# Kernel optimization log

Measured on AMD Instinct MI355X. Metric: run time of the kernel, lower is better.

## Reference

```python
import jax, jax.numpy as jnp
import numpy as np

# --- static config (matches init_kwargs) ---
B = 2; HI = 60; WI = 60; T = 4; WS = 8; SHIFT = 4
C = 256; NH = 8; HD = C // NH; HID = 1024
P = HI * WI; N = T * P
PAD = (WS - HI % WS) % WS           # 4 -> pad 60 -> 64
HP = HI + PAD; WP = WI + PAD
NWH = HP // WS; NWW = WP // WS
L = WS * WS                          # 64 tokens per window
SCALE = HD ** -0.5

# relative position index [L, L] (constant)
_c = np.stack(np.meshgrid(np.arange(WS), np.arange(WS), indexing='ij')).reshape(2, -1)
_r = (_c[:, :, None] - _c[:, None, :]).transpose(1, 2, 0) + WS - 1
REL_IDX = jnp.asarray(_r[..., 0] * (2 * WS - 1) + _r[..., 1])

# per-window key padding mask [nWin, L] (True = padded token)
_b = np.zeros((HP, WP), bool); _b[HI:, :] = True; _b[:, WI:] = True
WIN_MASK = jnp.asarray(_b.reshape(NWH, WS, NWW, WS).transpose(0, 2, 1, 3).reshape(NWH * NWW, L))


def _ln(x, w, b):
    m = x.mean(-1, keepdims=True)
    v = jnp.square(x - m).mean(-1, keepdims=True)
    return (x - m) * jax.lax.rsqrt(v + 1e-5) * w + b


def _partition(x4):  # [Bm, HP, WP, C] -> [Bm*nWin, L, C]
    Bm = x4.shape[0]
    return x4.reshape(Bm, NWH, WS, NWW, WS, C).transpose(0, 1, 3, 2, 4, 5).reshape(Bm * NWH * NWW, L, C)


def _win_attn(xq, xkv, qw, qb, kw, kb, vw, vb, ow, ob, bias_table):
    Bm = B * T
    q4 = xq.reshape(Bm, HI, WI, C)
    k4 = xkv.reshape(Bm, HI, WI, C)
    q4 = jnp.roll(q4, (-SHIFT, -SHIFT), (1, 2))
    k4 = jnp.roll(k4, (-SHIFT, -SHIFT), (1, 2))
    pad = ((0, 0), (0, PAD), (0, PAD), (0, 0))
    q4 = jnp.pad(q4, pad); k4 = jnp.pad(k4, pad)
    q_win = _partition(q4)   # [Bw, L, C]
    kv_win = _partition(k4)
    q = (q_win @ qw.T + qb).reshape(-1, L, NH, HD)
    k = (kv_win @ kw.T + kb).reshape(-1, L, NH, HD)
    v = (kv_win @ vw.T + vb).reshape(-1, L, NH, HD)
    attn = jnp.einsum('bihd,bjhd->bhij', q, k) * SCALE
    attn = attn + bias_table[REL_IDX].transpose(2, 0, 1)[None]      # RPB [1,H,L,L]
    km = jnp.tile(WIN_MASK, (Bm, 1))                                  # [Bw, L]
    attn = jnp.where(km[:, None, None, :], -jnp.inf, attn)
    p = jax.nn.softmax(attn, axis=-1)
    o = jnp.einsum('bhij,bjhd->bihd', p, v).reshape(-1, L, C)
    o = o @ ow.T + ob
    y = o.reshape(Bm, NWH, NWW, WS, WS, C).transpose(0, 1, 3, 2, 4, 5).reshape(Bm, HP, WP, C)
    y = y[:, :HI, :WI, :]
    y = jnp.roll(y, (SHIFT, SHIFT), (1, 2))
    return y.reshape(B, N, C)


def reference(x, context, ln1_w, ln1_b, ln2_w, ln2_b, ln3_w, ln3_b, lnc_w, lnc_b,
              sa_q_w, sa_q_b, sa_k_w, sa_k_b, sa_v_w, sa_v_b, sa_o_w, sa_o_b, sa_bias,
              ca_q_w, ca_q_b, ca_k_w, ca_k_b, ca_v_w, ca_v_b, ca_o_w, ca_o_b, ca_bias,
              gamma1, gamma2, gamma_mlp, mlp_w1, mlp_b1, mlp_w2, mlp_b2):
    xn = _ln(x, ln1_w, ln1_b)
    y_s = _win_attn(xn, xn, sa_q_w, sa_q_b, sa_k_w, sa_k_b, sa_v_w, sa_v_b, sa_o_w, sa_o_b, sa_bias)
    x = x + gamma1 * y_s
    y_c = _win_attn(_ln(x, ln2_w, ln2_b), _ln(context, lnc_w, lnc_b),
                    ca_q_w, ca_q_b, ca_k_w, ca_k_b, ca_v_w, ca_v_b, ca_o_w, ca_o_b, ca_bias)
    x = x + gamma2 * y_c
    h = _ln(x, ln3_w, ln3_b)
    h = jax.nn.gelu(h @ mlp_w1.T + mlp_b1, approximate=False) @ mlp_w2.T + mlp_b2
    return x + gamma_mlp * h


def setup_inputs() -> dict:
    key = jax.random.key(0)
    ks = jax.random.split(key, 16)
    def w(k, shape, s=0.02):
        return jax.random.normal(k, shape, jnp.float32) * s
    inp = {}
    inp['x'] = jax.random.normal(ks[0], (B, N, C), jnp.float32)
    inp['context'] = jax.random.normal(ks[1], (B, N, C), jnp.float32)
    for nm in ['ln1', 'ln2', 'ln3', 'lnc']:
        inp[f'{nm}_w'] = jnp.ones((C,), jnp.float32)
        inp[f'{nm}_b'] = jnp.zeros((C,), jnp.float32)
    i = 2
    for pfx in ['sa', 'ca']:
        for pn in ['q', 'k', 'v', 'o']:
            inp[f'{pfx}_{pn}_w'] = w(ks[i], (C, C)); i += 1
            inp[f'{pfx}_{pn}_b'] = jnp.zeros((C,), jnp.float32)
        inp[f'{pfx}_bias'] = w(ks[i], ((2 * WS - 1) * (2 * WS - 1), NH)); i += 1
    inp['gamma1'] = jnp.ones((1,), jnp.float32)
    inp['gamma2'] = jnp.ones((1,), jnp.float32)
    inp['gamma_mlp'] = jnp.full((1,), 0.1, jnp.float32)
    inp['mlp_w1'] = w(ks[i], (HID, C)); i += 1
    inp['mlp_b1'] = jnp.zeros((HID,), jnp.float32)
    inp['mlp_w2'] = w(ks[i], (C, HID)); i += 1
    inp['mlp_b2'] = jnp.zeros((C,), jnp.float32)
    return inp
```

## Files before the change

kernel.cpp:

```cpp
#include <hip/hip_runtime.h>
#include <math.h>

#define BN    28800
#define CC    256
#define HIDN  1024
#define WINS  512
#define WROWS (WINS*64)
#define ATT_SCALE 0.1767766952966369f

typedef __bf16 bf16x8 __attribute__((ext_vector_type(8)));
typedef float  f32x4  __attribute__((ext_vector_type(4)));

__device__ __forceinline__ unsigned short f2bf(float f) {
    unsigned u = __float_as_uint(f);
    unsigned r = (u + 0x7FFFu + ((u >> 16) & 1u)) >> 16;
    return (unsigned short)r;
}
__device__ __forceinline__ float bf2f(unsigned short u) {
    return __uint_as_float((unsigned)u << 16);
}

__device__ __forceinline__ float gelu_f(float x) {
    float x3 = x * x * x;
    float e  = __expf(1.5957691216057308f * (x + 0.044715f * x3));
    float th = 1.0f - 2.0f * __builtin_amdgcn_rcpf(e + 1.0f);
    return 0.5f * x * (1.0f + th);
}

__device__ __forceinline__ void gl_lds16(const void* g, void* l) {
    __builtin_amdgcn_global_load_lds(
        (const __attribute__((address_space(1))) void*)g,
        (__attribute__((address_space(3))) void*)l, 16, 0, 0);
}

__global__ void ln_gather(const float* __restrict__ x, const float* __restrict__ w,
                          const float* __restrict__ b, unsigned short* __restrict__ dst) {
    int row  = (int)((blockIdx.x * blockDim.x + threadIdx.x) >> 6);
    int lane = threadIdx.x & 63;
    if (row >= WROWS) return;
    int win = row >> 6, l = row & 63;
    int f   = win >> 6;
    int wih = (win >> 3) & 7, wiw = win & 7;
    int r = l >> 3, s = l & 7;
    int h = wih * 8 + r, wc = wiw * 8 + s;
    if (h >= 60 || wc >= 60) {
        ushort4 z = {0, 0, 0, 0};
        reinterpret_cast<ushort4*>(dst + (size_t)row * CC)[lane] = z;
        return;
    }
    int oh = (h + 4) % 60, ow = (wc + 4) % 60;
    size_t tok = (size_t)f * 3600 + (size_t)oh * 60 + ow;
    float4 v = reinterpret_cast<const float4*>(x + tok * CC)[lane];
    float sm  = v.x + v.y + v.z + v.w;
    float s2 = v.x*v.x + v.y*v.y + v.z*v.z + v.w*v.w;
#pragma unroll
    for (int off = 32; off >= 1; off >>= 1) {
        sm += __shfl_xor(sm, off);
        s2 += __shfl_xor(s2, off);
    }
    float mean = sm * (1.0f / CC);
    float var  = s2 * (1.0f / CC) - mean * mean;
    float rs   = rsqrtf(var + 1e-5f);
    float4 wv = reinterpret_cast<const float4*>(w)[lane];
    float4 bv = reinterpret_cast<const float4*>(b)[lane];
    ushort4 o;
    o.x = f2bf((v.x - mean) * rs * wv.x + bv.x);
    o.y = f2bf((v.y - mean) * rs * wv.y + bv.y);
    o.z = f2bf((v.z - mean) * rs * wv.z + bv.z);
    o.w = f2bf((v.w - mean) * rs * wv.w + bv.w);
    reinterpret_cast<ushort4*>(dst + (size_t)row * CC)[lane] = o;
}

template <bool GELU, int FUSE, int TN>
__global__ __launch_bounds__(512, 4) void gemm_wa(
        const unsigned short* __restrict__ Wt,
        const unsigned short* __restrict__ Act,
        const float* __restrict__ b0, const float* __restrict__ b1,
        const float* __restrict__ b2, const float* __restrict__ b3,
        unsigned short* __restrict__ o0, unsigned short* __restrict__ o1,
        unsigned short* __restrict__ o2, unsigned short* __restrict__ o3,
        int strideO, int vseg, int K, int Ntok,
        const float* __restrict__ xres, const float* __restrict__ gammap,
        float* __restrict__ fout) {
    constexpr int NW   = TN / 64;
    constexpr int BP   = TN / 128;
    constexpr int BUFB = 8192 + TN * 64;
    constexpr int POOLB = (3 * BUFB > TN * 256) ? 3 * BUFB : TN * 256;
    __shared__ __align__(16) char pool[POOLB];
    unsigned short* Cs = (unsigned short*)pool;

    const int t = threadIdx.x;
    const int w = t >> 6;
    const int l = t & 63;
    const int Mb = gridDim.x;
    int lin = blockIdx.y * Mb + blockIdx.x;
    int T = Mb * gridDim.y;
    int q = T >> 3, rr = T & 7;
    int xcd = lin & 7, slot = lin >> 3;
    int wid = (xcd < rr) ? (xcd * (q + 1) + slot)
                         : (rr * (q + 1) + (xcd - rr) * q + slot);
    const int m0 = (wid % Mb) * 128;
    const int n0 = (wid / Mb) * TN;

    const int wr = w >> 2, wc = w & 3;
    const int r = l & 15, g = l >> 4;
    const int gp = (g ^ ((r >> 1) & 3)) * 8;
    const int srow = t >> 2;
    const int sgl  = (t & 3) ^ ((srow >> 1) & 3);

    f32x4 acc[4][NW];
#pragma unroll
    for (int i = 0; i < 4; ++i)
#pragma unroll
        for (int j = 0; j < NW; ++j) { acc[i][j][0]=0.f; acc[i][j][1]=0.f; acc[i][j][2]=0.f; acc[i][j][3]=0.f; }

#define STAGE(k0, buf)                                                             \
    do {                                                                           \
        gl_lds16(Wt + (size_t)(m0 + srow) * K + (k0) + sgl * 8,                    \
                 pool + (buf) * BUFB + w * 1024);                                  \
        _Pragma("unroll")                                                          \
        for (int p = 0; p < BP; ++p) {                                             \
            int c    = p * 512 + t;                                                \
            int rowb = c >> 2;                                                     \
            int glb  = (c & 3) ^ ((rowb >> 1) & 3);                                \
            gl_lds16(Act + (size_t)(n0 + rowb) * K + (k0) + glb * 8,               \
                     pool + (buf) * BUFB + 8192 + p * 8192 + w * 1024);            \
        }                                                                          \
    } while (0)

    STAGE(0, 0);
    STAGE(32, 1);
    const char* cb0 = pool;
    const char* cb1 = pool + BUFB;
    const char* cb2 = pool + 2 * BUFB;
    int sbuf = 2;
    const int nt = K >> 5;
    for (int kt = 0; kt < nt; ++kt) {
        if (kt < nt - 1) {
            if (TN == 128) asm volatile("s_waitcnt vmcnt(2)" ::: "memory");
            else           asm volatile("s_waitcnt vmcnt(3)" ::: "memory");
        } else {
            asm volatile("s_waitcnt vmcnt(0)" ::: "memory");
        }
        __builtin_amdgcn_s_barrier();
        __builtin_amdgcn_sched_barrier(0);
        const unsigned short* cA = (const unsigned short*)cb0;
        const unsigned short* cB = (const unsigned short*)(cb0 + 8192);
        bf16x8 bw[NW];
#pragma unroll
        for (int n = 0; n < NW; ++n)
            bw[n] = *reinterpret_cast<const bf16x8*>(&cB[(wc * (NW * 16) + n * 16 + r) * 32 + gp]);
        __builtin_amdgcn_s_setprio(1);
#pragma unroll
        for (int m = 0; m < 4; ++m) {
            bf16x8 af = *reinterpret_cast<const bf16x8*>(&cA[(wr * 64 + m * 16 + r) * 32 + gp]);
#pragma unroll
            for (int n = 0; n < NW; ++n)
                acc[m][n] = __builtin_amdgcn_mfma_f32_16x16x32_bf16(af, bw[n], acc[m][n], 0, 0, 0);
        }
        __builtin_amdgcn_s_setprio(0);
        if (kt + 2 < nt) {
            STAGE((kt + 2) * 32, sbuf);
            sbuf = (sbuf == 2) ? 0 : sbuf + 1;
        }
        const char* tmp = cb0; cb0 = cb1; cb1 = cb2; cb2 = tmp;
    }
#undef STAGE

    const int seg = m0 >> 8;
    const float* bp = (seg == 0) ? b0 : (seg == 1) ? b1 : (seg == 2) ? b2 : b3;
    unsigned short* op = (seg == 0) ? o0 : (seg == 1) ? o1 : (seg == 2) ? o2 : o3;
    const int chseg = m0 & 255;

    if (FUSE == 0 && seg == vseg) {
#pragma unroll
        for (int m = 0; m < 4; ++m) {
            const int ch0 = chseg + wr * 64 + m * 16 + g * 4;
            float4 b4 = *reinterpret_cast<const float4*>(bp + ch0);
            const float bb[4] = {b4.x, b4.y, b4.z, b4.w};
#pragma unroll
            for (int n = 0; n < NW; ++n) {
                const int tok = n0 + wc * (NW * 16) + n * 16 + r;
#pragma unroll
                for (int j = 0; j < 4; ++j)
                    op[(size_t)(ch0 + j) * 32768 + tok] = f2bf(acc[m][n][j] + bb[j]);
            }
        }
        return;
    }

    __syncthreads();
#pragma unroll
    for (int m = 0; m < 4; ++m) {
        const int ch0 = wr * 64 + m * 16 + g * 4;
        float4 b4 = *reinterpret_cast<const float4*>(bp + chseg + ch0);
        const float bb[4] = {b4.x, b4.y, b4.z, b4.w};
#pragma unroll
        for (int n = 0; n < NW; ++n) {
            const int tok_l = wc * (NW * 16) + n * 16 + r;
            float cv[4];
#pragma unroll
            for (int j = 0; j < 4; ++j) {
                cv[j] = acc[m][n][j] + bb[j];
                if (GELU) cv[j] = gelu_f(cv[j]);
            }
            ushort4 pk;
            pk.x = f2bf(cv[0]); pk.y = f2bf(cv[1]); pk.z = f2bf(cv[2]); pk.w = f2bf(cv[3]);
            int gran = (ch0 >> 2) ^ ((tok_l & 15) << 1);
            reinterpret_cast<ushort4*>(Cs)[tok_l * 32 + gran] = pk;
        }
    }
    __syncthreads();
    const int u = t & 15, trow = t >> 4;
    if (FUSE == 0) {
#pragma unroll
        for (int it = 0; it < TN / 32; ++it) {
            int tok_l = it * 32 + trow;
            if (n0 + tok_l >= Ntok) continue;
            int up = u ^ (tok_l & 15);
            uint4 v = reinterpret_cast<const uint4*>(Cs)[tok_l * 16 + up];
            *reinterpret_cast<uint4*>(op + (size_t)(n0 + tok_l) * strideO + chseg + u * 8) = v;
        }
    } else {
        const float gsc = gammap[0];
#pragma unroll
        for (int it = 0; it < TN / 32; ++it) {
            int tok_l = it * 32 + trow;
            int wrow = n0 + tok_l;
            if (wrow >= Ntok) continue;
            int tok = wrow;
            int up = u ^ (tok_l & 15);
            uint4 v = reinterpret_cast<const uint4*>(Cs)[tok_l * 16 + up];
            const unsigned short* pu = (const unsigned short*)&v;
            const float* xr = xres + (size_t)tok * CC + chseg + u * 8;
            float4 xa = *reinterpret_cast<const float4*>(xr);
            float4 xb = *reinterpret_cast<const float4*>(xr + 4);
            float4 oa, ob;
            oa.x = xa.x + gsc * bf2f(pu[0]);
            oa.y = xa.y + gsc * bf2f(pu[1]);
            oa.z = xa.z + gsc * bf2f(pu[2]);
            oa.w = xa.w + gsc * bf2f(pu[3]);
            ob.x = xb.x + gsc * bf2f(pu[4]);
            ob.y = xb.y + gsc * bf2f(pu[5]);
            ob.z = xb.z + gsc * bf2f(pu[6]);
            ob.w = xb.w + gsc * bf2f(pu[7]);
            float* fo = fout + (size_t)tok * CC + chseg + u * 8;
            *reinterpret_cast<float4*>(fo) = oa;
            *reinterpret_cast<float4*>(fo + 4) = ob;
        }
    }
}

template <int LNM>
__global__ __launch_bounds__(512, 4) void gemm_ln(
        const unsigned short* __restrict__ Wt,
        const unsigned short* __restrict__ Act,
        const float* __restrict__ bias,
        const float* __restrict__ xres, const float* __restrict__ gammap,
        float* __restrict__ fout,
        const float* __restrict__ lnw, const float* __restrict__ lnb,
        unsigned short* __restrict__ lnout) {
    constexpr int BUFB = 16384 + 8192;
    __shared__ __align__(16) char pool[3 * BUFB];
    unsigned short* Cs = (unsigned short*)pool;

    const int t = threadIdx.x, w = t >> 6, l = t & 63;
    int lin = blockIdx.x;
    int T = gridDim.x;
    int q = T >> 3, rr = T & 7;
    int xcd = lin & 7, slot = lin >> 3;
    int wid = (xcd < rr) ? (xcd * (q + 1) + slot)
                         : (rr * (q + 1) + (xcd - rr) * q + slot);
    const int n0 = wid * 128;

    const int wr = w >> 2, wc = w & 3;
    const int r = l & 15, g = l >> 4;
    const int gp = (g ^ ((r >> 1) & 3)) * 8;
    const int K = 256;

    f32x4 acc[8][2];
#pragma unroll
    for (int i = 0; i < 8; ++i)
#pragma unroll
        for (int j = 0; j < 2; ++j) { acc[i][j][0]=0.f; acc[i][j][1]=0.f; acc[i][j][2]=0.f; acc[i][j][3]=0.f; }

#define STAGE(k0, buf)                                                             \
    do {                                                                           \
        _Pragma("unroll")                                                          \
        for (int p = 0; p < 2; ++p) {                                              \
            int c    = p * 512 + t;                                                \
            int rowa = c >> 2;                                                     \
            int gla  = (c & 3) ^ ((rowa >> 1) & 3);                                \
            gl_lds16(Wt + (size_t)rowa * K + (k0) + gla * 8,                       \
                     pool + (buf) * BUFB + (p * 512 + w * 64) * 16);               \
        }                                                                          \
        {                                                                          \
            int rowb = t >> 2;                                                     \
            int glb  = (t & 3) ^ ((rowb >> 1) & 3);                                \
            gl_lds16(Act + (size_t)(n0 + rowb) * K + (k0) + glb * 8,               \
                     pool + (buf) * BUFB + 16384 + w * 1024);                      \
        }                                                                          \
    } while (0)

    STAGE(0, 0);
    STAGE(32, 1);
    const char* cb0 = pool;
    const char* cb1 = pool + BUFB;
    const char* cb2 = pool + 2 * BUFB;
    int sbuf = 2;
    for (int kt = 0; kt < 8; ++kt) {
        if (kt < 7) asm volatile("s_waitcnt vmcnt(3)" ::: "memory");
        else        asm volatile("s_waitcnt vmcnt(0)" ::: "memory");
        __builtin_amdgcn_s_barrier();
        __builtin_amdgcn_sched_barrier(0);
        const unsigned short* cA = (const unsigned short*)cb0;
        const unsigned short* cB = (const unsigned short*)(cb0 + 16384);
        bf16x8 bw[2];
#pragma unroll
        for (int n = 0; n < 2; ++n)
            bw[n] = *reinterpret_cast<const bf16x8*>(&cB[(wc * 32 + n * 16 + r) * 32 + gp]);
        __builtin_amdgcn_s_setprio(1);
#pragma unroll
        for (int m = 0; m < 8; ++m) {
            bf16x8 af = *reinterpret_cast<const bf16x8*>(&cA[(wr * 128 + m * 16 + r) * 32 + gp]);
#pragma unroll
            for (int n = 0; n < 2; ++n)
                acc[m][n] = __builtin_amdgcn_mfma_f32_16x16x32_bf16(af, bw[n], acc[m][n], 0, 0, 0);
        }
        __builtin_amdgcn_s_setprio(0);
        if (kt + 2 < 8) {
            STAGE((kt + 2) * 32, sbuf);
            sbuf = (sbuf == 2) ? 0 : sbuf + 1;
        }
        const char* tmp = cb0; cb0 = cb1; cb1 = cb2; cb2 = tmp;
    }
#undef STAGE

    __syncthreads();
#pragma unroll
    for (int m = 0; m < 8; ++m) {
        const int ch0 = wr * 128 + m * 16 + g * 4;
        float4 b4 = *reinterpret_cast<const float4*>(bias + ch0);
        const float bb[4] = {b4.x, b4.y, b4.z, b4.w};
#pragma unroll
        for (int n = 0; n < 2; ++n) {
            const int tokh = wc * 32 + n * 16 + r;
            ushort4 pk;
            pk.x = f2bf(acc[m][n][0] + bb[0]);
            pk.y = f2bf(acc[m][n][1] + bb[1]);
            pk.z = f2bf(acc[m][n][2] + bb[2]);
            pk.w = f2bf(acc[m][n][3] + bb[3]);
            int gran = (ch0 >> 2) ^ ((tokh & 15) << 1);
            reinterpret_cast<ushort4*>(Cs)[tokh * 64 + gran] = pk;
        }
    }
    __syncthreads();

    const float gsc = gammap[0];
    const int u16 = t & 31, trow = t >> 5;
#pragma unroll
    for (int it = 0; it < 8; ++it) {
        int rowh = it * 16 + trow;
        int wrow = n0 + rowh;
        int win = wrow >> 6, l2 = wrow & 63;
        int f = win >> 6, wih = (win >> 3) & 7, wiw = win & 7;
        int r2 = l2 >> 3, s2 = l2 & 7;
        int hh = wih * 8 + r2, wcol = wiw * 8 + s2;
        bool pad = (hh >= 60) || (wcol >= 60);
        if (pad) {
            if (LNM == 1) {
                uint4 z = {0u, 0u, 0u, 0u};
                *reinterpret_cast<uint4*>(lnout + (size_t)wrow * CC + u16 * 8) = z;
            }
            continue;
        }
        int oh = hh + 4; if (oh >= 60) oh -= 60;
        int ow = wcol + 4; if (ow >= 60) ow -= 60;
        int tok = f * 3600 + oh * 60 + ow;

        int up = u16 ^ (rowh & 15);
        uint4 v = reinterpret_cast<const uint4*>(Cs)[rowh * 32 + up];
        const unsigned short* pu = (const unsigned short*)&v;
        const float* xr = xres + (size_t)tok * CC + u16 * 8;
        float4 xa = *reinterpret_cast<const float4*>(xr);
        float4 xb = *reinterpret_cast<const float4*>(xr + 4);
        float4 oa, ob;
        oa.x = xa.x + gsc * bf2f(pu[0]);
        oa.y = xa.y + gsc * bf2f(pu[1]);
        oa.z = xa.z + gsc * bf2f(pu[2]);
        oa.w = xa.w + gsc * bf2f(pu[3]);
        ob.x = xb.x + gsc * bf2f(pu[4]);
        ob.y = xb.y + gsc * bf2f(pu[5]);
        ob.z = xb.z + gsc * bf2f(pu[6]);
        ob.w = xb.w + gsc * bf2f(pu[7]);
        float* fo = fout + (size_t)tok * CC + u16 * 8;
        *reinterpret_cast<float4*>(fo) = oa;
        *reinterpret_cast<float4*>(fo + 4) = ob;

        float sm = oa.x + oa.y + oa.z + oa.w + ob.x + ob.y + ob.z + ob.w;
        float s2q = oa.x*oa.x + oa.y*oa.y + oa.z*oa.z + oa.w*oa.w
                  + ob.x*ob.x + ob.y*ob.y + ob.z*ob.z + ob.w*ob.w;
#pragma unroll
        for (int off = 1; off <= 16; off <<= 1) {
            sm  += __shfl_xor(sm, off);
            s2q += __shfl_xor(s2q, off);
        }
        float mean = sm * (1.0f / CC);
        float rs   = rsqrtf(s2q * (1.0f / CC) - mean * mean + 1e-5f);
        float4 w0 = *reinterpret_cast<const float4*>(lnw + u16 * 8);
        float4 w1 = *reinterpret_cast<const float4*>(lnw + u16 * 8 + 4);
        float4 c0 = *reinterpret_cast<const float4*>(lnb + u16 * 8);
        float4 c1 = *reinterpret_cast<const float4*>(lnb + u16 * 8 + 4);
        ushort4 pa, pb;
        pa.x = f2bf((oa.x - mean) * rs * w0.x + c0.x);
        pa.y = f2bf((oa.y - mean) * rs * w0.y + c0.y);
        pa.z = f2bf((oa.z - mean) * rs * w0.z + c0.z);
        pa.w = f2bf((oa.w - mean) * rs * w0.w + c0.w);
        pb.x = f2bf((ob.x - mean) * rs * w1.x + c1.x);
        pb.y = f2bf((ob.y - mean) * rs * w1.y + c1.y);
        pb.z = f2bf((ob.z - mean) * rs * w1.z + c1.z);
        pb.w = f2bf((ob.w - mean) * rs * w1.w + c1.w);
        size_t dst = (size_t)((LNM == 1) ? wrow : tok) * CC + u16 * 8;
        *reinterpret_cast<ushort4*>(lnout + dst)     = pa;
        *reinterpret_cast<ushort4*>(lnout + dst + 4) = pb;
    }
}

__global__ void expand_bias(const float* __restrict__ sa, const float* __restrict__ ca,
                            float* __restrict__ dst) {
    int e = (int)(blockIdx.x * blockDim.x + threadIdx.x);
    const float* src = (e < 16384) ? sa : ca;
    int e2 = e & 16383;
    int h = e2 >> 12, ij = e2 & 4095, i = ij >> 6, j = ij & 63;
    int ri = i >> 3, si = i & 7, rj = j >> 3, sj = j & 7;
    dst[e] = src[((ri - rj + 7) * 15 + (si - sj + 7)) * 8 + h];
}

__global__ __launch_bounds__(256) void attn_mfma(
        const unsigned short* __restrict__ Q,
        const unsigned short* __restrict__ K,
        const unsigned short* __restrict__ VT,
        const float* __restrict__ biasx,
        unsigned short* __restrict__ AO) {
    __shared__ __align__(16) unsigned short Pl[4][64 * 64];
    const int t = threadIdx.x;
    const int w = t >> 6, l = t & 63;
    const int win = blockIdx.x >> 1;
    const int h   = (blockIdx.x & 1) * 4 + w;
    const int c = l & 15, g = l >> 4;
    const int wih = (win >> 3) & 7, wiw = win & 7;
    const size_t qkbase = (size_t)win * 64 * CC + (size_t)h * 32;

    bf16x8 ka[4], qb[4];
#pragma unroll
    for (int mj = 0; mj < 4; ++mj)
        ka[mj] = *reinterpret_cast<const bf16x8*>(K + qkbase + (size_t)(mj * 16 + c) * CC + g * 8);
#pragma unroll
    for (int ni = 0; ni < 4; ++ni)
        qb[ni] = *reinterpret_cast<const bf16x8*>(Q + qkbase + (size_t)(ni * 16 + c) * CC + g * 8);
    f32x4 s[4][4];
#pragma unroll
    for (int mj = 0; mj < 4; ++mj)
#pragma unroll
        for (int ni = 0; ni < 4; ++ni) { s[mj][ni][0]=0.f; s[mj][ni][1]=0.f; s[mj][ni][2]=0.f; s[mj][ni][3]=0.f; }
#pragma unroll
    for (int mj = 0; mj < 4; ++mj)
#pragma unroll
        for (int ni = 0; ni < 4; ++ni)
            s[mj][ni] = __builtin_amdgcn_mfma_f32_16x16x32_bf16(ka[mj], qb[ni], s[mj][ni], 0, 0, 0);

    const float* bx = biasx + h * 4096;
    const bool modd = (wiw == 7) && (g & 1);
#pragma unroll
    for (int mj = 0; mj < 4; ++mj) {
        const bool mmj = (wih == 7) && (mj >= 2);
#pragma unroll
        for (int ni = 0; ni < 4; ++ni) {
            float4 b4 = *reinterpret_cast<const float4*>(bx + (ni * 16 + c) * 64 + mj * 16 + g * 4);
            const float bb[4] = {b4.x, b4.y, b4.z, b4.w};
#pragma unroll
            for (int jj = 0; jj < 4; ++jj) {
                float v = s[mj][ni][jj] * ATT_SCALE + bb[jj];
                s[mj][ni][jj] = (mmj || modd) ? -1e30f : v;
            }
        }
    }

#pragma unroll
    for (int ni = 0; ni < 4; ++ni) {
        float mx = -1e30f;
#pragma unroll
        for (int mj = 0; mj < 4; ++mj)
#pragma unroll
            for (int jj = 0; jj < 4; ++jj) mx = fmaxf(mx, s[mj][ni][jj]);
        mx = fmaxf(mx, __shfl_xor(mx, 16));
        mx = fmaxf(mx, __shfl_xor(mx, 32));
        float sum = 0.f;
#pragma unroll
        for (int mj = 0; mj < 4; ++mj)
#pragma unroll
            for (int jj = 0; jj < 4; ++jj) {
                float p = __expf(s[mj][ni][jj] - mx);
                s[mj][ni][jj] = p;
                sum += p;
            }
        sum += __shfl_xor(sum, 16);
        sum += __shfl_xor(sum, 32);
        float rinv = __builtin_amdgcn_rcpf(sum);
        const int i  = ni * 16 + c;
        const int ik = i & 7;
#pragma unroll
        for (int mj = 0; mj < 4; ++mj) {
            ushort4 pk;
            pk.x = f2bf(s[mj][ni][0] * rinv);
            pk.y = f2bf(s[mj][ni][1] * rinv);
            pk.z = f2bf(s[mj][ni][2] * rinv);
            pk.w = f2bf(s[mj][ni][3] * rinv);
            int chunk = (mj * 2 + (g >> 1)) ^ ik;
            *reinterpret_cast<ushort4*>((char*)&Pl[w][0] + i * 128 + chunk * 16 + (g & 1) * 8) = pk;
        }
    }

    bf16x8 vb[2][2];
#pragma unroll
    for (int nd = 0; nd < 2; ++nd)
#pragma unroll
        for (int kt = 0; kt < 2; ++kt)
            vb[nd][kt] = *reinterpret_cast<const bf16x8*>(
                VT + (size_t)(h * 32 + nd * 16 + c) * 32768 + win * 64 + kt * 32 + g * 8);
    f32x4 o[4][2];
#pragma unroll
    for (int mi = 0; mi < 4; ++mi)
#pragma unroll
        for (int nd = 0; nd < 2; ++nd) { o[mi][nd][0]=0.f; o[mi][nd][1]=0.f; o[mi][nd][2]=0.f; o[mi][nd][3]=0.f; }
#pragma unroll
    for (int mi = 0; mi < 4; ++mi) {
        const int i  = mi * 16 + c;
        const int ik = i & 7;
#pragma unroll
        for (int kt = 0; kt < 2; ++kt) {
            int chunk = (kt * 4 + g) ^ ik;
            bf16x8 pa = *reinterpret_cast<const bf16x8*>((char*)&Pl[w][0] + i * 128 + chunk * 16);
#pragma unroll
            for (int nd = 0; nd < 2; ++nd)
                o[mi][nd] = __builtin_amdgcn_mfma_f32_16x16x32_bf16(pa, vb[nd][kt], o[mi][nd], 0, 0, 0);
        }
    }

    unsigned short* aop = AO + qkbase;
#pragma unroll
    for (int mi = 0; mi < 4; ++mi)
#pragma unroll
        for (int nd = 0; nd < 2; ++nd)
#pragma unroll
            for (int jj = 0; jj < 4; ++jj)
                aop[(size_t)(mi * 16 + g * 4 + jj) * CC + nd * 16 + c] = f2bf(o[mi][nd][jj]);
}

__global__ void cvt_all(const float* s0, const float* s1, const float* s2, const float* s3,
                        const float* s4, const float* s5, const float* s6, const float* s7,
                        const float* s8, const float* s9, unsigned short* __restrict__ dst) {
    const float* srcs[10] = {s0, s1, s2, s3, s4, s5, s6, s7, s8, s9};
    int blk = blockIdx.x;
    int wi = (blk < 512) ? (blk >> 6) : (blk < 768 ? 8 : 9);
    size_t start = (wi < 8) ? (size_t)wi * 65536 : (wi == 8 ? (size_t)524288 : (size_t)786432);
    size_t gidx = (size_t)blk * 1024 + (size_t)threadIdx.x * 4;
    float4 v = *reinterpret_cast<const float4*>(srcs[wi] + (gidx - start));
    ushort4 o;
    o.x = f2bf(v.x); o.y = f2bf(v.y); o.z = f2bf(v.z); o.w = f2bf(v.w);
    *reinterpret_cast<ushort4*>(dst + gidx) = o;
}

extern "C" void kernel_launch(void* const* d_in, const int* in_sizes, int n_in,
                              void* d_out, int out_size, void* d_ws, size_t ws_size,
                              hipStream_t stream) {
    const float* x    = (const float*)d_in[0];
    const float* ctx  = (const float*)d_in[1];
    const float* ln1w = (const float*)d_in[2];
    const float* ln1b = (const float*)d_in[3];
    const float* ln2w = (const float*)d_in[4];
    const float* ln2b = (const float*)d_in[5];
    const float* ln3w = (const float*)d_in[6];
    const float* ln3b = (const float*)d_in[7];
    const float* lncw = (const float*)d_in[8];
    const float* lncb = (const float*)d_in[9];
    const float* saqw = (const float*)d_in[10];
    const float* saqb = (const float*)d_in[11];
    const float* sakw = (const float*)d_in[12];
    const float* sakb = (const float*)d_in[13];
    const float* savw = (const float*)d_in[14];
    const float* savb = (const float*)d_in[15];
    const float* saow = (const float*)d_in[16];
    const float* saob = (const float*)d_in[17];
    const float* sabias = (const float*)d_in[18];
    const float* caqw = (const float*)d_in[19];
    const float* caqb = (const float*)d_in[20];
    const float* cakw = (const float*)d_in[21];
    const float* cakb = (const float*)d_in[22];
    const float* cavw = (const float*)d_in[23];
    const float* cavb = (const float*)d_in[24];
    const float* caow = (const float*)d_in[25];
    const float* caob = (const float*)d_in[26];
    const float* cabias = (const float*)d_in[27];
    const float* gamma1 = (const float*)d_in[28];
    const float* gamma2 = (const float*)d_in[29];
    const float* gammam = (const float*)d_in[30];
    const float* mw1 = (const float*)d_in[31];
    const float* mb1 = (const float*)d_in[32];
    const float* mw2 = (const float*)d_in[33];
    const float* mb2 = (const float*)d_in[34];

    float* ws = (float*)d_ws;
    unsigned short* LNbf = (unsigned short*)(ws);
    unsigned short* Gq   = (unsigned short*)(ws + 3686400);
    unsigned short* Gkv  = (unsigned short*)(ws + 7880704);
    unsigned short* Qbf  = (unsigned short*)(ws + 12075008);
    unsigned short* Kbf  = (unsigned short*)(ws + 16269312);
    unsigned short* VTbf = (unsigned short*)(ws + 20463616);
    unsigned short* AObf = (unsigned short*)(ws + 24657920);
    float* X1  = ws + 28852224;
    unsigned short* Wp = (unsigned short*)(ws + 36225024);
    float* biasx = ws + 36749312;
    unsigned short* H1bf = Qbf;

    unsigned short* w_saqkv = Wp;
    unsigned short* w_sao   = Wp + 196608;
    unsigned short* w_caq   = Wp + 262144;
    unsigned short* w_cakv  = Wp + 327680;
    unsigned short* w_cao   = Wp + 458752;
    unsigned short* w_m1    = Wp + 524288;
    unsigned short* w_m2    = Wp + 786432;

    float* OUT = (float*)d_out;

    dim3 blk(256);
    dim3 blk512(512);
    dim3 gGather(WROWS / 4);
    dim3 gAttn(WINS * 2);

    cvt_all<<<dim3(1024), blk, 0, stream>>>(saqw, sakw, savw, saow, caqw, cakw, cavw, caow, mw1, mw2, Wp);
    expand_bias<<<dim3(128), blk, 0, stream>>>(sabias, cabias, biasx);

    ln_gather<<<gGather, blk, 0, stream>>>(x, ln1w, ln1b, Gq);
    gemm_wa<false,0,256><<<dim3(6, 128), blk512, 0, stream>>>(w_saqkv, Gq, saqb, sakb, savb, savb,
                                                              Qbf, Kbf, VTbf, VTbf, CC, 2, CC, WROWS,
                                                              nullptr, nullptr, nullptr);
    attn_mfma<<<gAttn, blk, 0, stream>>>(Qbf, Kbf, VTbf, biasx, AObf);
    gemm_ln<1><<<dim3(256), blk512, 0, stream>>>(w_sao, AObf, saob, x, gamma1, X1, ln2w, ln2b, Gq);

    ln_gather<<<gGather, blk, 0, stream>>>(ctx, lncw, lncb, Gkv);
    gemm_wa<false,0,128><<<dim3(2, 256), blk512, 0, stream>>>(w_caq, Gq, caqb, caqb, caqb, caqb,
                                                              Qbf, Qbf, Qbf, Qbf, CC, -1, CC, WROWS,
                                                              nullptr, nullptr, nullptr);
    gemm_wa<false,0,256><<<dim3(4, 128), blk512, 0, stream>>>(w_cakv, Gkv, cakb, cavb, cavb, cavb,
                                                              Kbf, VTbf, VTbf, VTbf, CC, 1, CC, WROWS,
                                                              nullptr, nullptr, nullptr);
    attn_mfma<<<gAttn, blk, 0, stream>>>(Qbf, Kbf, VTbf, biasx + 16384, AObf);
    gemm_ln<2><<<dim3(256), blk512, 0, stream>>>(w_cao, AObf, caob, X1, gamma2, X1, ln3w, ln3b, LNbf);

    gemm_wa<true,0,256><<<dim3(8, 113), blk512, 0, stream>>>(w_m1, LNbf, mb1, mb1 + 256, mb1 + 512, mb1 + 768,
                                                             H1bf, H1bf + 256, H1bf + 512, H1bf + 768,
                                                             HIDN, -1, CC, BN, nullptr, nullptr, nullptr);
    gemm_wa<false,2,256><<<dim3(2, 113), blk512, 0, stream>>>(w_m2, H1bf, mb2, mb2, mb2, mb2,
                                                             Qbf, Qbf, Qbf, Qbf, CC, -1, HIDN, BN,
                                                             X1, gammam, OUT);
}
```

Measured before the change: 225.1 us.

## Merge launches, fuse cross-attn QKV GEMMs, stage attention output via LDS

Folds the weight conversion and bias expansion into one kernel and the two LN-gather passes into one launch. The cross-attention Q and KV projections now run as a single GEMM that picks its activation source per segment. Attention output is staged through shared memory so it can be written to global memory as coalesced 16-byte stores. The MLP second GEMM moves to a narrower 128-wide token tile with more blocks. Together these cut launch count and scattered stores, at the cost of extra LDS synchronisation in the attention epilogue and a different tile shape for the last GEMM.

```diff
diff --git a/kernel.cpp b/kernel.cpp
--- a/kernel.cpp
+++ b/kernel.cpp
@@ -33,24 +33,31 @@
         (__attribute__((address_space(3))) void*)l, 16, 0, 0);
 }
 
-__global__ void ln_gather(const float* __restrict__ x, const float* __restrict__ w,
-                          const float* __restrict__ b, unsigned short* __restrict__ dst) {
-    int row  = (int)((blockIdx.x * blockDim.x + threadIdx.x) >> 6);
+__global__ void ln_gather2(const float* __restrict__ x,   const float* __restrict__ w1,
+                           const float* __restrict__ b1,  unsigned short* __restrict__ d1,
+                           const float* __restrict__ ctx, const float* __restrict__ wc,
+                           const float* __restrict__ bc,  unsigned short* __restrict__ d2) {
+    const int half = blockIdx.x >> 13;
+    const float* src = half ? ctx : x;
+    const float* w   = half ? wc  : w1;
+    const float* b   = half ? bc  : b1;
+    unsigned short* dst = half ? d2 : d1;
+    int row  = (int)((((blockIdx.x & 8191) * blockDim.x) + threadIdx.x) >> 6);
     int lane = threadIdx.x & 63;
     if (row >= WROWS) return;
     int win = row >> 6, l = row & 63;
     int f   = win >> 6;
     int wih = (win >> 3) & 7, wiw = win & 7;
     int r = l >> 3, s = l & 7;
-    int h = wih * 8 + r, wc = wiw * 8 + s;
-    if (h >= 60 || wc >= 60) {
+    int h = wih * 8 + r, wc2 = wiw * 8 + s;
+    if (h >= 60 || wc2 >= 60) {
         ushort4 z = {0, 0, 0, 0};
         reinterpret_cast<ushort4*>(dst + (size_t)row * CC)[lane] = z;
         return;
     }
-    int oh = (h + 4) % 60, ow = (wc + 4) % 60;
+    int oh = (h + 4) % 60, ow = (wc2 + 4) % 60;
     size_t tok = (size_t)f * 3600 + (size_t)oh * 60 + ow;
-    float4 v = reinterpret_cast<const float4*>(x + tok * CC)[lane];
+    float4 v = reinterpret_cast<const float4*>(src + tok * CC)[lane];
     float sm  = v.x + v.y + v.z + v.w;
     float s2 = v.x*v.x + v.y*v.y + v.z*v.z + v.w*v.w;
 #pragma unroll
@@ -74,7 +81,9 @@
 template <bool GELU, int FUSE, int TN>
 __global__ __launch_bounds__(512, 4) void gemm_wa(
         const unsigned short* __restrict__ Wt,
-        const unsigned short* __restrict__ Act,
+        const unsigned short* __restrict__ a0c,
+        const unsigned short* __restrict__ a1c,
+        const unsigned short* __restrict__ a2c,
         const float* __restrict__ b0, const float* __restrict__ b1,
         const float* __restrict__ b2, const float* __restrict__ b3,
         unsigned short* __restrict__ o0, unsigned short* __restrict__ o1,
@@ -102,6 +111,9 @@
     const int m0 = (wid % Mb) * 128;
     const int n0 = (wid / Mb) * TN;
 
+    const int seg = m0 >> 8;
+    const unsigned short* Act = (seg == 0) ? a0c : (seg == 1) ? a1c : a2c;
+
     const int wr = w >> 2, wc = w & 3;
     const int r = l & 15, g = l >> 4;
     const int gp = (g ^ ((r >> 1) & 3)) * 8;
@@ -167,7 +179,6 @@
     }
 #undef STAGE
 
-    const int seg = m0 >> 8;
     const float* bp = (seg == 0) ? b0 : (seg == 1) ? b1 : (seg == 2) ? b2 : b3;
     unsigned short* op = (seg == 0) ? o0 : (seg == 1) ? o1 : (seg == 2) ? o2 : o3;
     const int chseg = m0 & 255;
@@ -426,16 +437,6 @@
     }
 }
 
-__global__ void expand_bias(const float* __restrict__ sa, const float* __restrict__ ca,
-                            float* __restrict__ dst) {
-    int e = (int)(blockIdx.x * blockDim.x + threadIdx.x);
-    const float* src = (e < 16384) ? sa : ca;
-    int e2 = e & 16383;
-    int h = e2 >> 12, ij = e2 & 4095, i = ij >> 6, j = ij & 63;
-    int ri = i >> 3, si = i & 7, rj = j >> 3, sj = j & 7;
-    dst[e] = src[((ri - rj + 7) * 15 + (si - sj + 7)) * 8 + h];
-}
-
 __global__ __launch_bounds__(256) void attn_mfma(
         const unsigned short* __restrict__ Q,
         const unsigned short* __restrict__ K,
@@ -547,21 +548,42 @@
         }
     }
 
-    unsigned short* aop = AO + qkbase;
+    unsigned short* AOs = &Pl[0][0];
+    __syncthreads();
 #pragma unroll
     for (int mi = 0; mi < 4; ++mi)
 #pragma unroll
         for (int nd = 0; nd < 2; ++nd)
 #pragma unroll
             for (int jj = 0; jj < 4; ++jj)
-                aop[(size_t)(mi * 16 + g * 4 + jj) * CC + nd * 16 + c] = f2bf(o[mi][nd][jj]);
-}
-
-__global__ void cvt_all(const float* s0, const float* s1, const float* s2, const float* s3,
-                        const float* s4, const float* s5, const float* s6, const float* s7,
-                        const float* s8, const float* s9, unsigned short* __restrict__ dst) {
+                AOs[(mi * 16 + g * 4 + jj) * 136 + w * 32 + nd * 16 + c] = f2bf(o[mi][nd][jj]);
+    __syncthreads();
+    unsigned short* aop = AO + (size_t)win * 64 * CC + (blockIdx.x & 1) * 128;
+    const int u = t & 15, rr2 = t >> 4;
+#pragma unroll
+    for (int it = 0; it < 4; ++it) {
+        int row = it * 16 + rr2;
+        uint4 v = *reinterpret_cast<const uint4*>(&AOs[row * 136 + u * 8]);
+        *reinterpret_cast<uint4*>(aop + (size_t)row * CC + u * 8) = v;
+    }
+}
+
+__global__ void cvt_bias(const float* s0, const float* s1, const float* s2, const float* s3,
+                         const float* s4, const float* s5, const float* s6, const float* s7,
+                         const float* s8, const float* s9, unsigned short* __restrict__ dst,
+                         const float* __restrict__ sa, const float* __restrict__ ca,
+                         float* __restrict__ biasx) {
+    int blk = blockIdx.x;
+    if (blk >= 1024) {
+        int e = (blk - 1024) * 256 + threadIdx.x;
+        const float* src = (e < 16384) ? sa : ca;
+        int e2 = e & 16383;
+        int h = e2 >> 12, ij = e2 & 4095, i = ij >> 6, j = ij & 63;
+        int ri = i >> 3, si = i & 7, rj = j >> 3, sj = j & 7;
+        biasx[e] = src[((ri - rj + 7) * 15 + (si - sj + 7)) * 8 + h];
+        return;
+    }
     const float* srcs[10] = {s0, s1, s2, s3, s4, s5, s6, s7, s8, s9};
-    int blk = blockIdx.x;
     int wi = (blk < 512) ? (blk >> 6) : (blk < 768 ? 8 : 9);
     size_t start = (wi < 8) ? (size_t)wi * 65536 : (wi == 8 ? (size_t)524288 : (size_t)786432);
     size_t gidx = (size_t)blk * 1024 + (size_t)threadIdx.x * 4;
@@ -625,8 +647,7 @@
 
     unsigned short* w_saqkv = Wp;
     unsigned short* w_sao   = Wp + 196608;
-    unsigned short* w_caq   = Wp + 262144;
-    unsigned short* w_cakv  = Wp + 327680;
+    unsigned short* w_caqkv = Wp + 262144;
     unsigned short* w_cao   = Wp + 458752;
     unsigned short* w_m1    = Wp + 524288;
     unsigned short* w_m2    = Wp + 786432;
@@ -635,33 +656,32 @@
 
     dim3 blk(256);
     dim3 blk512(512);
-    dim3 gGather(WROWS / 4);
     dim3 gAttn(WINS * 2);
 
-    cvt_all<<<dim3(1024), blk, 0, stream>>>(saqw, sakw, savw, saow, caqw, cakw, cavw, caow, mw1, mw2, Wp);
-    expand_bias<<<dim3(128), blk, 0, stream>>>(sabias, cabias, biasx);
-
-    ln_gather<<<gGather, blk, 0, stream>>>(x, ln1w, ln1b, Gq);
-    gemm_wa<false,0,256><<<dim3(6, 128), blk512, 0, stream>>>(w_saqkv, Gq, saqb, sakb, savb, savb,
+    cvt_bias<<<dim3(1152), blk, 0, stream>>>(saqw, sakw, savw, saow, caqw, cakw, cavw, caow,
+                                             mw1, mw2, Wp, sabias, cabias, biasx);
+    ln_gather2<<<dim3(16384), blk, 0, stream>>>(x, ln1w, ln1b, Gq, ctx, lncw, lncb, Gkv);
+
+    gemm_wa<false,0,256><<<dim3(6, 128), blk512, 0, stream>>>(w_saqkv, Gq, Gq, Gq,
+                                                              saqb, sakb, savb, savb,
                                                               Qbf, Kbf, VTbf, VTbf, CC, 2, CC, WROWS,
                                                               nullptr, nullptr, nullptr);
     attn_mfma<<<gAttn, blk, 0, stream>>>(Qbf, Kbf, VTbf, biasx, AObf);
     gemm_ln<1><<<dim3(256), blk512, 0, stream>>>(w_sao, AObf, saob, x, gamma1, X1, ln2w, ln2b, Gq);
 
-    ln_gather<<<gGather, blk, 0, stream>>>(ctx, lncw, lncb, Gkv);
-    gemm_wa<false,0,128><<<dim3(2, 256), blk512, 0, stream>>>(w_caq, Gq, caqb, caqb, caqb, caqb,
-                                                              Qbf, Qbf, Qbf, Qbf, CC, -1, CC, WROWS,
-                                                              nullptr, nullptr, nullptr);
-    gemm_wa<false,0,256><<<dim3(4, 128), blk512, 0, stream>>>(w_cakv, Gkv, cakb, cavb, cavb, cavb,
-                                                              Kbf, VTbf, VTbf, VTbf, CC, 1, CC, WROWS,
+    gemm_wa<false,0,256><<<dim3(6, 128), blk512, 0, stream>>>(w_caqkv, Gq, Gkv, Gkv,
+                                                              caqb, cakb, cavb, cavb,
+                                                              Qbf, Kbf, VTbf, VTbf, CC, 2, CC, WROWS,
                                                               nullptr, nullptr, nullptr);
     attn_mfma<<<gAttn, blk, 0, stream>>>(Qbf, Kbf, VTbf, biasx + 16384, AObf);
     gemm_ln<2><<<dim3(256), blk512, 0, stream>>>(w_cao, AObf, caob, X1, gamma2, X1, ln3w, ln3b, LNbf);
 
-    gemm_wa<true,0,256><<<dim3(8, 113), blk512, 0, stream>>>(w_m1, LNbf, mb1, mb1 + 256, mb1 + 512, mb1 + 768,
+    gemm_wa<true,0,256><<<dim3(8, 113), blk512, 0, stream>>>(w_m1, LNbf, LNbf, LNbf,
+                                                             mb1, mb1 + 256, mb1 + 512, mb1 + 768,
                                                              H1bf, H1bf + 256, H1bf + 512, H1bf + 768,
                                                              HIDN, -1, CC, BN, nullptr, nullptr, nullptr);
-    gemm_wa<false,2,256><<<dim3(2, 113), blk512, 0, stream>>>(w_m2, H1bf, mb2, mb2, mb2, mb2,
+    gemm_wa<false,2,128><<<dim3(2, 225), blk512, 0, stream>>>(w_m2, H1bf, H1bf, H1bf,
+                                                             mb2, mb2, mb2, mb2,
                                                              Qbf, Qbf, Qbf, Qbf, CC, -1, HIDN, BN,
                                                              X1, gammam, OUT);
 }
```

Result: faster. 213.8 us (median of 2 runs) (-5.0%).
